# Kernel optimization log

Measured on AMD Instinct MI355X. Metric: run time of the kernel, lower is better.

## Reference

```python
import jax, jax.numpy as jnp
import numpy as np

B, C, N, F_, HID = 512, 3, 128, 256, 128  # batch, channels, nodes(=in_dim), num_f(=seq), gru hidden


def setup_inputs() -> dict:
    key = jax.random.key(0)
    ks = jax.random.split(key, 12)
    s = 0.05
    inp = {
        "X": jax.random.normal(ks[0], (B, N, F_), jnp.float32),
        "H": jax.random.uniform(ks[1], (B, C, N, N), jnp.float32),
        "weight": jnp.full((1, 1), 10.0, jnp.float32),        # nn.init.constant_(weight, 10)
        "soft": jnp.full((C,), 1.0 / C, jnp.float32),          # nn.init.constant_(soft, 1/C)
        "w_ih_f": jax.random.normal(ks[2], (3 * HID, N), jnp.float32) * s,
        "w_hh_f": jax.random.normal(ks[3], (3 * HID, HID), jnp.float32) * s,
        "b_ih_f": jax.random.normal(ks[4], (3 * HID,), jnp.float32) * s,
        "b_hh_f": jax.random.normal(ks[5], (3 * HID,), jnp.float32) * s,
        "w_ih_b": jax.random.normal(ks[6], (3 * HID, N), jnp.float32) * s,
        "w_hh_b": jax.random.normal(ks[7], (3 * HID, HID), jnp.float32) * s,
        "b_ih_b": jax.random.normal(ks[8], (3 * HID,), jnp.float32) * s,
        "b_hh_b": jax.random.normal(ks[9], (3 * HID,), jnp.float32) * s,
        "bn_gamma": jnp.ones((F_,), jnp.float32),
        "bn_beta": jnp.zeros((F_,), jnp.float32),
    }
    return inp


def _gru_dir(xs, w_ih, w_hh, b_ih, b_hh):
    # xs: [T, B, in] -> ys: [T, B, HID]; torch GRU cell equations
    def cell(h, x):
        gi = x @ w_ih.T + b_ih
        gh = h @ w_hh.T + b_hh
        i_r, i_z, i_n = jnp.split(gi, 3, axis=-1)
        h_r, h_z, h_n = jnp.split(gh, 3, axis=-1)
        r = jax.nn.sigmoid(i_r + h_r)
        z = jax.nn.sigmoid(i_z + h_z)
        n = jnp.tanh(i_n + r * h_n)
        h_new = (1.0 - z) * n + z * h
        return h_new, h_new
    h0 = jnp.zeros((xs.shape[1], w_hh.shape[1]), xs.dtype)
    _, ys = jax.lax.scan(cell, h0, xs)
    return ys


def reference(X, H, weight, soft, w_ih_f, w_hh_f, b_ih_f, b_hh_f,
              w_ih_b, w_hh_b, b_ih_b, b_hh_b, bn_gamma, bn_beta):
    n = X.shape[1]
    I = jnp.eye(n, dtype=X.dtype)
    # norm(): zero the diagonal, add identity, symmetric D^-1/2 H D^-1/2 (all C channels at once)
    Hn = H * (1.0 - I) + I                              # [B,C,N,N]
    deg = jnp.sum(Hn, axis=-1)                          # [B,C,N]
    dinv = deg ** -0.5
    Hn = dinv[..., :, None] * Hn * dinv[..., None, :]
    # gcn_conv across all features/channels in one einsum; weight is a 1x1 scalar
    HX = jnp.einsum('bcnm,bmf->bcnf', Hn, X) * weight[0, 0]
    Xc = jnp.sum(jax.nn.leaky_relu(HX, 0.01) * soft[None, :, None, None], axis=1)  # [B,N,F]
    # per1 -> [B, F, N]; GRU batch_first with seq_len=F, input=N
    xs = Xc.transpose(2, 0, 1)                          # [T=F, B, N]
    yf = _gru_dir(xs, w_ih_f, w_hh_f, b_ih_f, b_hh_f)
    yb = _gru_dir(xs[::-1], w_ih_b, w_hh_b, b_ih_b, b_hh_b)[::-1]
    y = jnp.concatenate([yf, yb], axis=-1).transpose(1, 0, 2)  # [B, F, 2*HID]

    # BatchNorm1d(num_f), training-mode batch stats over (batch, length) per channel F
    mean = jnp.mean(y, axis=(0, 2), keepdims=True)
    var = jnp.var(y, axis=(0, 2), keepdims=True)
    y = bn_gamma[None, :, None] * (y - mean) / jnp.sqrt(var + 1e-5) + bn_beta[None, :, None]
    # per2 -> [B, 2*HID, F]
    return y.transpose(0, 2, 1)
```

## Files before the change

### kernel.cpp

```cpp
#include <hip/hip_runtime.h>

typedef short s8v  __attribute__((ext_vector_type(8)));
typedef float f4v  __attribute__((ext_vector_type(4)));

#define B_   512
#define C_   3
#define N_   128
#define F_   256
#define T_   256
#define HID_ 128
#define G3_  384

__device__ __forceinline__ ushort f2bf(float f) {
  union { float f; unsigned u; } v; v.f = f;
  return (ushort)((v.u + 0x7FFFu + ((v.u >> 16) & 1u)) >> 16);
}
__device__ __forceinline__ float bf2f(ushort h) {
  union { unsigned u; float f; } v; v.u = ((unsigned)h) << 16;
  return v.f;
}
__device__ __forceinline__ float rcp_(float x) { return __builtin_amdgcn_rcpf(x); }
__device__ __forceinline__ float sigm(float x) { return rcp_(1.0f + __expf(-x)); }
__device__ __forceinline__ float tanh_(float x) { return 2.0f * rcp_(1.0f + __expf(-2.0f * x)) - 1.0f; }

__global__ void k_wcvt(const float* __restrict__ a, const float* __restrict__ b,
                       const float* __restrict__ c, const float* __restrict__ d,
                       ushort* __restrict__ o) {
  int i = blockIdx.x * 256 + threadIdx.x;
  const float* src = (i < 49152) ? a : (i < 98304) ? b : (i < 147456) ? c : d;
  o[i] = f2bf(src[i % 49152]);
}

__global__ void k_dinv(const float* __restrict__ H, float* __restrict__ dinv) {
  const int bc = blockIdx.x;
  const int lane = threadIdx.x & 63, w = threadIdx.x >> 6;
  const float* Hm = H + (size_t)bc * N_ * N_;
  for (int r = w * 32; r < w * 32 + 32; ++r) {
    float a = Hm[(size_t)r * N_ + lane];
    float b = Hm[(size_t)r * N_ + 64 + lane];
    if (lane == r) a = 1.0f;
    if (64 + lane == r) b = 1.0f;
    float s = a + b;
    #pragma unroll
    for (int o = 32; o; o >>= 1) s += __shfl_xor(s, o);
    if (lane == 0) dinv[bc * N_ + r] = 1.0f / sqrtf(s);
  }
}

__global__ __launch_bounds__(256, 1) void k_conv(
    const float* __restrict__ X, const float* __restrict__ H,
    const float* __restrict__ dinv, const float* __restrict__ wscal,
    const float* __restrict__ soft, ushort* __restrict__ XcT) {
  __shared__ ushort hn[C_][N_][136];
  __shared__ ushort xt[N_][136];
  __shared__ float dv[C_ * N_];
  const int b = blockIdx.x;
  const int tid = threadIdx.x;
  const int lane = tid & 63, w = tid >> 6;
  const int rq = lane >> 4, l15 = lane & 15;

  for (int i = tid; i < C_ * N_; i += 256) dv[i] = dinv[b * C_ * N_ + i];
  __syncthreads();

  {
    const int m4 = (tid & 31) * 4;
    const int nof = tid >> 5;
    for (int c = 0; c < C_; ++c) {
      const float* Hm = H + ((size_t)(b * C_ + c)) * N_ * N_;
      const float* dvc = dv + c * N_;
      #pragma unroll
      for (int p = 0; p < 16; ++p) {
        int n = p * 8 + nof;
        float4 v = *(const float4*)&Hm[(size_t)n * N_ + m4];
        float f0 = (m4 + 0 == n) ? 1.0f : v.x;
        float f1 = (m4 + 1 == n) ? 1.0f : v.y;
        float f2 = (m4 + 2 == n) ? 1.0f : v.z;
        float f3 = (m4 + 3 == n) ? 1.0f : v.w;
        ushort4 o;
        o.x = f2bf(f0 * dvc[m4 + 0]);
        o.y = f2bf(f1 * dvc[m4 + 1]);
        o.z = f2bf(f2 * dvc[m4 + 2]);
        o.w = f2bf(f3 * dvc[m4 + 3]);
        *(ushort4*)&hn[c][n][m4] = o;
      }
    }
  }

  const float wmul = wscal[0];
  const float scf[3] = {soft[0], soft[1], soft[2]};

  for (int fh = 0; fh < 2; ++fh) {
    __syncthreads();
    {
      const int fl4 = (tid & 31) * 4;
      const int mof = tid >> 5;
      #pragma unroll
      for (int p = 0; p < 16; ++p) {
        int m = p * 8 + mof;
        float4 v = *(const float4*)&X[((size_t)b * N_ + m) * F_ + fh * 128 + fl4];
        xt[fl4 + 0][m] = f2bf(v.x);
        xt[fl4 + 1][m] = f2bf(v.y);
        xt[fl4 + 2][m] = f2bf(v.z);
        xt[fl4 + 3][m] = f2bf(v.w);
      }
    }
    __syncthreads();

    s8v af[2][4];
    #pragma unroll
    for (int rt = 0; rt < 2; ++rt)
      #pragma unroll
      for (int kk = 0; kk < 4; ++kk)
        af[rt][kk] = *(const s8v*)&xt[w * 32 + rt * 16 + l15][kk * 32 + rq * 8];

    f4v xc[2][8];
    #pragma unroll
    for (int rt = 0; rt < 2; ++rt)
      #pragma unroll
      for (int nt = 0; nt < 8; ++nt)
        xc[rt][nt] = (f4v){0.f, 0.f, 0.f, 0.f};

    for (int c = 0; c < C_; ++c) {
      f4v hx[2][8];
      #pragma unroll
      for (int rt = 0; rt < 2; ++rt)
        #pragma unroll
        for (int nt = 0; nt < 8; ++nt)
          hx[rt][nt] = (f4v){0.f, 0.f, 0.f, 0.f};
      #pragma unroll
      for (int kk = 0; kk < 4; ++kk) {
        #pragma unroll
        for (int nt = 0; nt < 8; ++nt) {
          s8v bf = *(const s8v*)&hn[c][nt * 16 + l15][kk * 32 + rq * 8];
          hx[0][nt] = __builtin_amdgcn_mfma_f32_16x16x32_bf16(af[0][kk], bf, hx[0][nt], 0, 0, 0);
          hx[1][nt] = __builtin_amdgcn_mfma_f32_16x16x32_bf16(af[1][kk], bf, hx[1][nt], 0, 0, 0);
        }
      }
      const float* dvc = dv + c * N_;
      const float s = scf[c];
      #pragma unroll
      for (int nt = 0; nt < 8; ++nt) {
        float dn = dvc[nt * 16 + l15] * wmul;
        #pragma unroll
        for (int i = 0; i < 4; ++i) {
          float v0 = hx[0][nt][i] * dn;
          xc[0][nt][i] += s * fmaxf(v0, 0.01f * v0);
          float v1 = hx[1][nt][i] * dn;
          xc[1][nt][i] += s * fmaxf(v1, 0.01f * v1);
        }
      }
    }
    __syncthreads();
    #pragma unroll
    for (int rt = 0; rt < 2; ++rt)
      #pragma unroll
      for (int nt = 0; nt < 8; ++nt)
        #pragma unroll
        for (int i = 0; i < 4; ++i)
          xt[w * 32 + rt * 16 + rq * 4 + i][nt * 16 + l15] = f2bf(xc[rt][nt][i]);
    __syncthreads();
    #pragma unroll
    for (int p = 0; p < 4; ++p) {
      int tl = p * 32 + (tid >> 3);
      int n0 = (tid & 7) * 16;
      size_t rowb = ((size_t)b * F_ + fh * 128 + tl) * N_;
      *(s8v*)&XcT[rowb + n0]     = *(const s8v*)&xt[tl][n0];
      *(s8v*)&XcT[rowb + n0 + 8] = *(const s8v*)&xt[tl][n0 + 8];
    }
  }
}

__global__ __launch_bounds__(512, 2) void k_gru(
    const ushort* __restrict__ XcT, const ushort* __restrict__ wbf,
    const float* __restrict__ bihf, const float* __restrict__ bhhf,
    const float* __restrict__ bihb, const float* __restrict__ bhhb,
    ushort* __restrict__ y) {
  __shared__ ushort hlds[2][16][136];
  __shared__ ushort xbuf[2][16][136];
  const int dir = blockIdx.x >> 5;
  const int chunk = blockIdx.x & 31;
  const int tid = threadIdx.x;
  const int lane = tid & 63, w = tid >> 6;
  const int rq = lane >> 4, l15 = lane & 15;
  const int g = w * 16 + l15;
  const ushort* wih = wbf + (size_t)(dir * 2) * G3_ * HID_;
  const ushort* whh = wih + G3_ * HID_;
  const float* bih = dir ? bihb : bihf;
  const float* bhh = dir ? bhhb : bhhf;

  s8v fir[4], fiz[4], fin[4], fhr[4], fhz[4], fhn[4];
  #pragma unroll
  for (int kk = 0; kk < 4; ++kk) {
    const int ko = kk * 32 + rq * 8;
    fir[kk] = *(const s8v*)&wih[(size_t)(g)       * HID_ + ko];
    fiz[kk] = *(const s8v*)&wih[(size_t)(128 + g) * HID_ + ko];
    fin[kk] = *(const s8v*)&wih[(size_t)(256 + g) * HID_ + ko];
    fhr[kk] = *(const s8v*)&whh[(size_t)(g)       * HID_ + ko];
    fhz[kk] = *(const s8v*)&whh[(size_t)(128 + g) * HID_ + ko];
    fhn[kk] = *(const s8v*)&whh[(size_t)(256 + g) * HID_ + ko];
  }
  const float b_r  = bih[g] + bhh[g];
  const float b_z  = bih[128 + g] + bhh[128 + g];
  const float b_in = bih[256 + g];
  const float b_hn = bhh[256 + g];

  for (int i = tid; i < 16 * 136; i += 512) ((ushort*)hlds[0])[i] = 0;

  const int rr = tid >> 5;
  const int nq = (tid & 31) * 4;
  const size_t xrow = (size_t)(chunk * 16 + rr) * T_;
  {
    int t0 = dir ? (T_ - 1) : 0;
    *(ushort4*)&xbuf[0][rr][nq] = *(const ushort4*)&XcT[(xrow + t0) * N_ + nq];
  }
  float hreg[4] = {0.f, 0.f, 0.f, 0.f};
  __syncthreads();

  for (int s = 0; s < T_; ++s) {
    const int cur = s & 1;
    const int t_in = dir ? (T_ - 1 - s) : s;
    const int sn = (s + 1 < T_) ? s + 1 : s;
    const int t_nx = dir ? (T_ - 1 - sn) : sn;
    ushort4 xn = *(const ushort4*)&XcT[(xrow + t_nx) * N_ + nq];

    f4v ar  = {b_r, b_r, b_r, b_r};
    f4v az  = {b_z, b_z, b_z, b_z};
    f4v ain = {b_in, b_in, b_in, b_in};
    f4v ahn = {b_hn, b_hn, b_hn, b_hn};
    #pragma unroll
    for (int kk = 0; kk < 4; ++kk) {
      const int ko = kk * 32 + rq * 8;
      s8v xf = *(const s8v*)&xbuf[cur][l15][ko];
      s8v hf = *(const s8v*)&hlds[cur][l15][ko];
      ar  = __builtin_amdgcn_mfma_f32_16x16x32_bf16(xf, fir[kk], ar, 0, 0, 0);
      ar  = __builtin_amdgcn_mfma_f32_16x16x32_bf16(hf, fhr[kk], ar, 0, 0, 0);
      az  = __builtin_amdgcn_mfma_f32_16x16x32_bf16(xf, fiz[kk], az, 0, 0, 0);
      az  = __builtin_amdgcn_mfma_f32_16x16x32_bf16(hf, fhz[kk], az, 0, 0, 0);
      ain = __builtin_amdgcn_mfma_f32_16x16x32_bf16(xf, fin[kk], ain, 0, 0, 0);
      ahn = __builtin_amdgcn_mfma_f32_16x16x32_bf16(hf, fhn[kk], ahn, 0, 0, 0);
    }
    ushort hb[4];
    #pragma unroll
    for (int i = 0; i < 4; ++i) {
      float r = sigm(ar[i]);
      float z = sigm(az[i]);
      float n = tanh_(ain[i] + r * ahn[i]);
      float h = n + z * (hreg[i] - n);
      hreg[i] = h;
      hb[i] = f2bf(h);
    }
    ushort4 hv; hv.x = hb[0]; hv.y = hb[1]; hv.z = hb[2]; hv.w = hb[3];
    *(ushort4*)&y[((size_t)t_in * 256 + dir * 128 + g) * B_ + chunk * 16 + rq * 4] = hv;
    hlds[cur ^ 1][rq * 4 + 0][g] = hb[0];
    hlds[cur ^ 1][rq * 4 + 1][g] = hb[1];
    hlds[cur ^ 1][rq * 4 + 2][g] = hb[2];
    hlds[cur ^ 1][rq * 4 + 3][g] = hb[3];
    *(ushort4*)&xbuf[cur ^ 1][rr][nq] = xn;
    __syncthreads();
  }
}

__global__ void k_stats(const ushort* __restrict__ y, const float* __restrict__ gamma,
                        const float* __restrict__ beta, float* __restrict__ stats) {
  const int t = blockIdx.x, tid = threadIdx.x;
  const ushort* p = y + (size_t)t * 256 * B_;
  float s = 0.f, q = 0.f;
  for (int i = tid * 8; i < 256 * B_; i += 256 * 8) {
    s8v v = *(const s8v*)&p[i];
    #pragma unroll
    for (int e = 0; e < 8; ++e) {
      float f = bf2f((ushort)v[e]);
      s += f; q += f * f;
    }
  }
  #pragma unroll
  for (int o = 32; o; o >>= 1) { s += __shfl_xor(s, o); q += __shfl_xor(q, o); }
  __shared__ float rs[4], rq2[4];
  if ((tid & 63) == 0) { rs[tid >> 6] = s; rq2[tid >> 6] = q; }
  __syncthreads();
  if (tid == 0) {
    s = rs[0] + rs[1] + rs[2] + rs[3];
    q = rq2[0] + rq2[1] + rq2[2] + rq2[3];
    const float inv = 1.0f / (256.f * 512.f);
    float mean = s * inv;
    float var = q * inv - mean * mean;
    float istd = 1.0f / sqrtf(var + 1e-5f);
    float a = gamma[t] * istd;
    stats[2 * t] = a;
    stats[2 * t + 1] = beta[t] - mean * a;
  }
}

__global__ __launch_bounds__(256) void k_apply(
    const ushort* __restrict__ y, const float* __restrict__ stats,
    float* __restrict__ out) {
  __shared__ ushort tile[64][264];
  __shared__ float sA[256], sB[256];
  const int j = blockIdx.x;
  const int b0 = blockIdx.y * 64;
  const int tid = threadIdx.x;
  sA[tid] = stats[2 * tid];
  sB[tid] = stats[2 * tid + 1];
  const int tof = tid >> 4;
  const int boff = (tid & 15) * 4;
  #pragma unroll
  for (int p = 0; p < 16; ++p) {
    int t = p * 16 + tof;
    ushort4 v = *(const ushort4*)&y[((size_t)t * 256 + j) * B_ + b0 + boff];
    tile[boff + 0][t] = v.x;
    tile[boff + 1][t] = v.y;
    tile[boff + 2][t] = v.z;
    tile[boff + 3][t] = v.w;
  }
  __syncthreads();
  const int bb = tid >> 2;
  const int tq = (tid & 3) * 64;
  float* op = out + ((size_t)(b0 + bb) * 256 + j) * 256 + tq;
  for (int k = 0; k < 64; k += 8) {
    s8v v = *(const s8v*)&tile[bb][tq + k];
    float4 o0, o1;
    o0.x = bf2f((ushort)v[0]) * sA[tq + k + 0] + sB[tq + k + 0];
    o0.y = bf2f((ushort)v[1]) * sA[tq + k + 1] + sB[tq + k + 1];
    o0.z = bf2f((ushort)v[2]) * sA[tq + k + 2] + sB[tq + k + 2];
    o0.w = bf2f((ushort)v[3]) * sA[tq + k + 3] + sB[tq + k + 3];
    o1.x = bf2f((ushort)v[4]) * sA[tq + k + 4] + sB[tq + k + 4];
    o1.y = bf2f((ushort)v[5]) * sA[tq + k + 5] + sB[tq + k + 5];
    o1.z = bf2f((ushort)v[6]) * sA[tq + k + 6] + sB[tq + k + 6];
    o1.w = bf2f((ushort)v[7]) * sA[tq + k + 7] + sB[tq + k + 7];
    *(float4*)&op[k] = o0;
    *(float4*)&op[k + 4] = o1;
  }
}

extern "C" void kernel_launch(void* const* d_in, const int* in_sizes, int n_in,
                              void* d_out, int out_size, void* d_ws, size_t ws_size,
                              hipStream_t stream) {
  const float* X      = (const float*)d_in[0];
  const float* H      = (const float*)d_in[1];
  const float* weight = (const float*)d_in[2];
  const float* soft   = (const float*)d_in[3];
  const float* w_ih_f = (const float*)d_in[4];
  const float* w_hh_f = (const float*)d_in[5];
  const float* b_ih_f = (const float*)d_in[6];
  const float* b_hh_f = (const float*)d_in[7];
  const float* w_ih_b = (const float*)d_in[8];
  const float* w_hh_b = (const float*)d_in[9];
  const float* b_ih_b = (const float*)d_in[10];
  const float* b_hh_b = (const float*)d_in[11];
  const float* gamma  = (const float*)d_in[12];
  const float* beta   = (const float*)d_in[13];
  float* out = (float*)d_out;

  char* ws = (char*)d_ws;
  ushort* wbf   = (ushort*)(ws);
  float*  dinv  = (float*) (ws + 393216);
  ushort* XcT   = (ushort*)(ws + 1179648);
  ushort* ybuf  = (ushort*)(ws + 34734080);
  float*  stats = (float*) (ws + 101842944);

  k_wcvt<<<768, 256, 0, stream>>>(w_ih_f, w_hh_f, w_ih_b, w_hh_b, wbf);
  k_dinv<<<B_ * C_, 256, 0, stream>>>(H, dinv);
  k_conv<<<B_, 256, 0, stream>>>(X, H, dinv, weight, soft, XcT);
  k_gru<<<64, 512, 0, stream>>>(XcT, wbf, b_ih_f, b_hh_f, b_ih_b, b_hh_b, ybuf);
  k_stats<<<T_, 256, 0, stream>>>(ybuf, gamma, beta, stats);
  k_apply<<<dim3(256, 8), 256, 0, stream>>>(ybuf, stats, out);
}
```

Measured before the change: 409.9 us.

## Transpose GRU MFMA operands, change y layout to [T,B,256], cheaper barrier

The GRU MFMA operands are swapped so each lane holds four consecutive hidden units for one batch row. Hidden state can then be written to LDS and global memory as single ushort4 stores, and y is stored as [T][B][256]. The per-step __syncthreads is replaced by an inline lgkmcnt wait plus s_barrier, which avoids waiting on outstanding global stores. k_apply is reorganised around the new y layout with an XOR-swizzled LDS tile, and k_stats still sums per T, so it stays valid under the new layout. The risk is that the asm barrier does not order global memory, which is acceptable here because only LDS is shared between steps.

```diff
diff --git a/kernel.cpp b/kernel.cpp
--- a/kernel.cpp
+++ b/kernel.cpp
@@ -22,6 +22,8 @@
 __device__ __forceinline__ float rcp_(float x) { return __builtin_amdgcn_rcpf(x); }
 __device__ __forceinline__ float sigm(float x) { return rcp_(1.0f + __expf(-x)); }
 __device__ __forceinline__ float tanh_(float x) { return 2.0f * rcp_(1.0f + __expf(-2.0f * x)) - 1.0f; }
+
+#define LDS_BARRIER() asm volatile("s_waitcnt lgkmcnt(0)\n\ts_barrier" ::: "memory")
 
 __global__ void k_wcvt(const float* __restrict__ a, const float* __restrict__ b,
                        const float* __restrict__ c, const float* __restrict__ d,
@@ -182,7 +184,8 @@
   const int tid = threadIdx.x;
   const int lane = tid & 63, w = tid >> 6;
   const int rq = lane >> 4, l15 = lane & 15;
-  const int g = w * 16 + l15;
+  const int jb = w * 16;
+  const int jr = jb + rq * 4;
   const ushort* wih = wbf + (size_t)(dir * 2) * G3_ * HID_;
   const ushort* whh = wih + G3_ * HID_;
   const float* bih = dir ? bihb : bihf;
@@ -192,17 +195,22 @@
   #pragma unroll
   for (int kk = 0; kk < 4; ++kk) {
     const int ko = kk * 32 + rq * 8;
-    fir[kk] = *(const s8v*)&wih[(size_t)(g)       * HID_ + ko];
-    fiz[kk] = *(const s8v*)&wih[(size_t)(128 + g) * HID_ + ko];
-    fin[kk] = *(const s8v*)&wih[(size_t)(256 + g) * HID_ + ko];
-    fhr[kk] = *(const s8v*)&whh[(size_t)(g)       * HID_ + ko];
-    fhz[kk] = *(const s8v*)&whh[(size_t)(128 + g) * HID_ + ko];
-    fhn[kk] = *(const s8v*)&whh[(size_t)(256 + g) * HID_ + ko];
-  }
-  const float b_r  = bih[g] + bhh[g];
-  const float b_z  = bih[128 + g] + bhh[128 + g];
-  const float b_in = bih[256 + g];
-  const float b_hn = bhh[256 + g];
+    const int row = jb + l15;
+    fir[kk] = *(const s8v*)&wih[(size_t)(row)       * HID_ + ko];
+    fiz[kk] = *(const s8v*)&wih[(size_t)(128 + row) * HID_ + ko];
+    fin[kk] = *(const s8v*)&wih[(size_t)(256 + row) * HID_ + ko];
+    fhr[kk] = *(const s8v*)&whh[(size_t)(row)       * HID_ + ko];
+    fhz[kk] = *(const s8v*)&whh[(size_t)(128 + row) * HID_ + ko];
+    fhn[kk] = *(const s8v*)&whh[(size_t)(256 + row) * HID_ + ko];
+  }
+  float4 bi_r = *(const float4*)&bih[jr],        bh_r = *(const float4*)&bhh[jr];
+  float4 bi_z = *(const float4*)&bih[128 + jr],  bh_z = *(const float4*)&bhh[128 + jr];
+  float4 bin4 = *(const float4*)&bih[256 + jr];
+  float4 bhn4 = *(const float4*)&bhh[256 + jr];
+  f4v br = {bi_r.x + bh_r.x, bi_r.y + bh_r.y, bi_r.z + bh_r.z, bi_r.w + bh_r.w};
+  f4v bz = {bi_z.x + bh_z.x, bi_z.y + bh_z.y, bi_z.z + bh_z.z, bi_z.w + bh_z.w};
+  f4v bin = {bin4.x, bin4.y, bin4.z, bin4.w};
+  f4v bhn = {bhn4.x, bhn4.y, bhn4.z, bhn4.w};
 
   for (int i = tid; i < 16 * 136; i += 512) ((ushort*)hlds[0])[i] = 0;
 
@@ -213,7 +221,7 @@
     int t0 = dir ? (T_ - 1) : 0;
     *(ushort4*)&xbuf[0][rr][nq] = *(const ushort4*)&XcT[(xrow + t0) * N_ + nq];
   }
-  float hreg[4] = {0.f, 0.f, 0.f, 0.f};
+  f4v hreg = {0.f, 0.f, 0.f, 0.f};
   __syncthreads();
 
   for (int s = 0; s < T_; ++s) {
@@ -223,21 +231,18 @@
     const int t_nx = dir ? (T_ - 1 - sn) : sn;
     ushort4 xn = *(const ushort4*)&XcT[(xrow + t_nx) * N_ + nq];
 
-    f4v ar  = {b_r, b_r, b_r, b_r};
-    f4v az  = {b_z, b_z, b_z, b_z};
-    f4v ain = {b_in, b_in, b_in, b_in};
-    f4v ahn = {b_hn, b_hn, b_hn, b_hn};
+    f4v ar = br, az = bz, ain = bin, ahn = bhn;
     #pragma unroll
     for (int kk = 0; kk < 4; ++kk) {
       const int ko = kk * 32 + rq * 8;
       s8v xf = *(const s8v*)&xbuf[cur][l15][ko];
       s8v hf = *(const s8v*)&hlds[cur][l15][ko];
-      ar  = __builtin_amdgcn_mfma_f32_16x16x32_bf16(xf, fir[kk], ar, 0, 0, 0);
-      ar  = __builtin_amdgcn_mfma_f32_16x16x32_bf16(hf, fhr[kk], ar, 0, 0, 0);
-      az  = __builtin_amdgcn_mfma_f32_16x16x32_bf16(xf, fiz[kk], az, 0, 0, 0);
-      az  = __builtin_amdgcn_mfma_f32_16x16x32_bf16(hf, fhz[kk], az, 0, 0, 0);
-      ain = __builtin_amdgcn_mfma_f32_16x16x32_bf16(xf, fin[kk], ain, 0, 0, 0);
-      ahn = __builtin_amdgcn_mfma_f32_16x16x32_bf16(hf, fhn[kk], ahn, 0, 0, 0);
+      ar  = __builtin_amdgcn_mfma_f32_16x16x32_bf16(fir[kk], xf, ar, 0, 0, 0);
+      ar  = __builtin_amdgcn_mfma_f32_16x16x32_bf16(fhr[kk], hf, ar, 0, 0, 0);
+      az  = __builtin_amdgcn_mfma_f32_16x16x32_bf16(fiz[kk], xf, az, 0, 0, 0);
+      az  = __builtin_amdgcn_mfma_f32_16x16x32_bf16(fhz[kk], hf, az, 0, 0, 0);
+      ain = __builtin_amdgcn_mfma_f32_16x16x32_bf16(fin[kk], xf, ain, 0, 0, 0);
+      ahn = __builtin_amdgcn_mfma_f32_16x16x32_bf16(fhn[kk], hf, ahn, 0, 0, 0);
     }
     ushort hb[4];
     #pragma unroll
@@ -250,13 +255,10 @@
       hb[i] = f2bf(h);
     }
     ushort4 hv; hv.x = hb[0]; hv.y = hb[1]; hv.z = hb[2]; hv.w = hb[3];
-    *(ushort4*)&y[((size_t)t_in * 256 + dir * 128 + g) * B_ + chunk * 16 + rq * 4] = hv;
-    hlds[cur ^ 1][rq * 4 + 0][g] = hb[0];
-    hlds[cur ^ 1][rq * 4 + 1][g] = hb[1];
-    hlds[cur ^ 1][rq * 4 + 2][g] = hb[2];
-    hlds[cur ^ 1][rq * 4 + 3][g] = hb[3];
+    *(ushort4*)&y[((size_t)t_in * B_ + chunk * 16 + l15) * 256 + dir * 128 + jr] = hv;
+    *(ushort4*)&hlds[cur ^ 1][l15][jr] = hv;
     *(ushort4*)&xbuf[cur ^ 1][rr][nq] = xn;
-    __syncthreads();
+    LDS_BARRIER();
   }
 }
 
@@ -294,41 +296,37 @@
 __global__ __launch_bounds__(256) void k_apply(
     const ushort* __restrict__ y, const float* __restrict__ stats,
     float* __restrict__ out) {
-  __shared__ ushort tile[64][264];
+  __shared__ ushort tile[256][64];
   __shared__ float sA[256], sB[256];
-  const int j = blockIdx.x;
-  const int b0 = blockIdx.y * 64;
+  const int b = blockIdx.x;
+  const int j0 = blockIdx.y * 64;
   const int tid = threadIdx.x;
   sA[tid] = stats[2 * tid];
   sB[tid] = stats[2 * tid + 1];
-  const int tof = tid >> 4;
-  const int boff = (tid & 15) * 4;
+  {
+    const ushort* src = &y[((size_t)tid * B_ + b) * 256 + j0];
+    const int sw = (tid >> 5) & 7;
+    #pragma unroll
+    for (int q = 0; q < 8; ++q)
+      *(s8v*)&tile[tid][(q ^ sw) * 8] = *(const s8v*)&src[q * 8];
+  }
+  __syncthreads();
+  const int j = tid >> 2, jc = j >> 3, jrr = j & 7;
+  const int tq = tid & 3;
+  float* op = out + ((size_t)b * 256 + j0 + j) * 256 + tq * 64;
   #pragma unroll
-  for (int p = 0; p < 16; ++p) {
-    int t = p * 16 + tof;
-    ushort4 v = *(const ushort4*)&y[((size_t)t * 256 + j) * B_ + b0 + boff];
-    tile[boff + 0][t] = v.x;
-    tile[boff + 1][t] = v.y;
-    tile[boff + 2][t] = v.z;
-    tile[boff + 3][t] = v.w;
-  }
-  __syncthreads();
-  const int bb = tid >> 2;
-  const int tq = (tid & 3) * 64;
-  float* op = out + ((size_t)(b0 + bb) * 256 + j) * 256 + tq;
-  for (int k = 0; k < 64; k += 8) {
-    s8v v = *(const s8v*)&tile[bb][tq + k];
-    float4 o0, o1;
-    o0.x = bf2f((ushort)v[0]) * sA[tq + k + 0] + sB[tq + k + 0];
-    o0.y = bf2f((ushort)v[1]) * sA[tq + k + 1] + sB[tq + k + 1];
-    o0.z = bf2f((ushort)v[2]) * sA[tq + k + 2] + sB[tq + k + 2];
-    o0.w = bf2f((ushort)v[3]) * sA[tq + k + 3] + sB[tq + k + 3];
-    o1.x = bf2f((ushort)v[4]) * sA[tq + k + 4] + sB[tq + k + 4];
-    o1.y = bf2f((ushort)v[5]) * sA[tq + k + 5] + sB[tq + k + 5];
-    o1.z = bf2f((ushort)v[6]) * sA[tq + k + 6] + sB[tq + k + 6];
-    o1.w = bf2f((ushort)v[7]) * sA[tq + k + 7] + sB[tq + k + 7];
-    *(float4*)&op[k] = o0;
-    *(float4*)&op[k + 4] = o1;
+  for (int k = 0; k < 16; ++k) {
+    const int t = tq * 64 + k * 4;
+    float4 o;
+    #pragma unroll
+    for (int e = 0; e < 4; ++e) {
+      const int te = t + e;
+      const int sw2 = (te >> 5) & 7;
+      const int jcol = ((jc ^ sw2) * 8) + jrr;
+      float vv = bf2f(tile[te][jcol]) * sA[te] + sB[te];
+      if (e == 0) o.x = vv; else if (e == 1) o.y = vv; else if (e == 2) o.z = vv; else o.w = vv;
+    }
+    *(float4*)&op[k * 4] = o;
   }
 }
 
@@ -363,5 +361,5 @@
   k_conv<<<B_, 256, 0, stream>>>(X, H, dinv, weight, soft, XcT);
   k_gru<<<64, 512, 0, stream>>>(XcT, wbf, b_ih_f, b_hh_f, b_ih_b, b_hh_b, ybuf);
   k_stats<<<T_, 256, 0, stream>>>(ybuf, gamma, beta, stats);
-  k_apply<<<dim3(256, 8), 256, 0, stream>>>(ybuf, stats, out);
-}
+  k_apply<<<dim3(512, 4), 256, 0, stream>>>(ybuf, stats, out);
+}
```

Measured after the change: 403.4 us. No clear change (-1.6%).
